# Optimization experiments

Hardware: AMD Instinct MI355X
Metric: run time of the kernel (lower is better)

## Reference

```python
import jax, jax.numpy as jnp
import numpy as np

B, S, D, H = 2, 2048, 1024, 16
HD = D // H
SCALE = float(np.sqrt(HD))


def setup_inputs() -> dict:
    key = jax.random.key(0)
    ks = jax.random.split(key, 11)
    std = 1.0 / np.sqrt(D)
    inp = {
        "query": jax.random.normal(ks[0], (B, S, D), dtype=jnp.float32),
        "key": jax.random.normal(ks[1], (B, S, D), dtype=jnp.float32),
        "value": jax.random.normal(ks[2], (B, S, D), dtype=jnp.float32),
        "w_q": jax.random.normal(ks[3], (D, D), dtype=jnp.float32) * std,
        "b_q": jax.random.normal(ks[4], (D,), dtype=jnp.float32) * std,
        "w_k": jax.random.normal(ks[5], (D, D), dtype=jnp.float32) * std,
        "b_k": jax.random.normal(ks[6], (D,), dtype=jnp.float32) * std,
        "w_v": jax.random.normal(ks[7], (D, D), dtype=jnp.float32) * std,
        "b_v": jax.random.normal(ks[8], (D,), dtype=jnp.float32) * std,
        "w_fc": jax.random.normal(ks[9], (D, D), dtype=jnp.float32) * std,
        "b_fc": jax.random.normal(ks[10], (D,), dtype=jnp.float32) * std,
    }
    return inp


def reference(query, key, value, w_q, b_q, w_k, b_k, w_v, b_v, w_fc, b_fc):
    # Linear projections (torch Linear: x @ W^T + b; here w_* stored as [in, out])
    Q = query @ w_q + b_q            # [B, S, D]
    K = key @ w_k + b_k
    V = value @ w_v + b_v
    # split heads -> [B, H, S, HD]
    Q = Q.reshape(B, S, H, HD).transpose(0, 2, 1, 3)
    K = K.reshape(B, S, H, HD).transpose(0, 2, 1, 3)
    V = V.reshape(B, S, H, HD).transpose(0, 2, 1, 3)
    energy = jnp.einsum('bhqd,bhkd->bhqk', Q, K) / SCALE  # [B, H, S, S]
    attn = jax.nn.softmax(energy, axis=-1)
    x = jnp.einsum('bhqk,bhkd->bhqd', attn, V)            # [B, H, S, HD]
    x = x.transpose(0, 2, 1, 3).reshape(B, S, D)
    return x @ w_fc + b_fc
```

## Files before the change

kernel.cpp:

```cpp
#include <hip/hip_runtime.h>
#include <stdint.h>

#define Bz 2
#define Sz 2048
#define Dz 1024
#define Hz 16
#define HDz 64
#define Mz (Bz*Sz)

typedef unsigned short u16;
typedef __attribute__((ext_vector_type(8))) __bf16 bf16x8;
typedef __attribute__((ext_vector_type(8))) unsigned short u16x8;
typedef __attribute__((ext_vector_type(4))) float f32x4;

#define C1 0.1803368801111243f

__device__ __forceinline__ u16 f2bf(float f) {
  union { float f; unsigned u; } v; v.f = f;
  unsigned r = v.u + 0x7fffu + ((v.u >> 16) & 1u);
  return (u16)(r >> 16);
}

__device__ __forceinline__ void async16(void* lds, const void* g) {
  __builtin_amdgcn_global_load_lds(
      (const __attribute__((address_space(1))) unsigned int*)g,
      (__attribute__((address_space(3))) unsigned int*)lds, 16, 0, 0);
}

__global__ void cvt3_kernel(const float* __restrict__ q, const float* __restrict__ k,
                            const float* __restrict__ v,
                            u16* __restrict__ xq, u16* __restrict__ xk, u16* __restrict__ xv,
                            int n4) {
  const float* in = blockIdx.y == 0 ? q : blockIdx.y == 1 ? k : v;
  u16* out = blockIdx.y == 0 ? xq : blockIdx.y == 1 ? xk : xv;
  int i = blockIdx.x * blockDim.x + threadIdx.x;
  if (i < n4) {
    float4 t = ((const float4*)in)[i];
    ((ushort4*)out)[i] = make_ushort4(f2bf(t.x), f2bf(t.y), f2bf(t.z), f2bf(t.w));
  }
}

__global__ void wt_cvt_kernel(const float* __restrict__ w0, const float* __restrict__ w1,
                              const float* __restrict__ w2, const float* __restrict__ w3,
                              u16* __restrict__ Wt ) {
  const float* W = blockIdx.z == 0 ? w0 : blockIdx.z == 1 ? w1 : blockIdx.z == 2 ? w2 : w3;
  u16* o = Wt + (size_t)blockIdx.z * Dz * Dz;
  __shared__ __align__(16) float t[32][33];
  int n0 = blockIdx.x * 32, k0 = blockIdx.y * 32;
  int x = threadIdx.x, y = threadIdx.y;
#pragma unroll
  for (int i = 0; i < 4; ++i)
    t[y + i*8][x] = W[(size_t)(k0 + y + i*8) * Dz + n0 + x];
  __syncthreads();
#pragma unroll
  for (int i = 0; i < 4; ++i)
    o[(size_t)(n0 + y + i*8) * Dz + k0 + x] = f2bf(t[x][y + i*8]);
}

__global__ void __launch_bounds__(256)
vtrans_kernel(const u16* __restrict__ Vp, u16* __restrict__ Vt) {
  __shared__ __align__(16) u16 t[64][72];
  int s0 = blockIdx.x * 64, bh = blockIdx.y;
  int b = bh >> 4;
  int h = bh & 15;
  int tid = threadIdx.x;
#pragma unroll
  for (int p = 0; p < 4; ++p) {
    int c = p * 256 + tid;
    int row = c >> 4, off = (c & 15) * 4;
    ushort4 v = *(const ushort4*)(Vp + (size_t)(b * Sz + s0 + row) * Dz + h * 64 + off);
    *(ushort4*)&t[row][off] = v;
  }
  __syncthreads();
#pragma unroll
  for (int p = 0; p < 4; ++p) {
    int c = p * 256 + tid;
    int d = c >> 4, sc = (c & 15) * 4;
    ushort4 v = make_ushort4(t[sc + 0][d], t[sc + 1][d], t[sc + 2][d], t[sc + 3][d]);
    *(ushort4*)(Vt + (size_t)(bh * 64 + d) * Sz + s0 + sc) = v;
  }
}

__global__ void __launch_bounds__(256)
gemm_qkv(const u16* __restrict__ xq, const u16* __restrict__ xk, const u16* __restrict__ xv,
         const u16* __restrict__ Wt3,
         const float* __restrict__ bq, const float* __restrict__ bk, const float* __restrict__ bv,
         u16* __restrict__ Qp, u16* __restrict__ Kp, u16* __restrict__ Vp)
{
  __shared__ __align__(16) u16 lA[128][32];
  __shared__ __align__(16) u16 lB[128][32];
  const int sel = blockIdx.x >> 3;
  const int n0 = (blockIdx.x & 7) * 128;
  const int m0 = blockIdx.y * 128;
  const u16* A = sel == 0 ? xq : sel == 1 ? xk : xv;
  const u16* Bt = Wt3 + (size_t)sel * Dz * Dz;
  const float* bias = sel == 0 ? bq : sel == 1 ? bk : bv;
  u16* Cv = sel == 0 ? Qp : sel == 1 ? Kp : Vp;

  const int tid = threadIdx.x;
  const int w = tid >> 6, lane = tid & 63;
  const int wm = (w >> 1) * 64, wn = (w & 1) * 64;
  const int l16 = lane & 15, qd = lane >> 4;

  f32x4 acc[4][4];
#pragma unroll
  for (int i = 0; i < 4; ++i)
#pragma unroll
    for (int j = 0; j < 4; ++j) acc[i][j] = (f32x4){0.f, 0.f, 0.f, 0.f};

  const int r0 = tid >> 2, c0 = (tid & 3) * 8;
  const int r1 = r0 + 64;

  for (int k0 = 0; k0 < Dz; k0 += 32) {
    __syncthreads();
    async16(&lA[r0][c0], A  + (size_t)(m0 + r0) * Dz + k0 + c0);
    async16(&lB[r0][c0], Bt + (size_t)(n0 + r0) * Dz + k0 + c0);
    async16(&lA[r1][c0], A  + (size_t)(m0 + r1) * Dz + k0 + c0);
    async16(&lB[r1][c0], Bt + (size_t)(n0 + r1) * Dz + k0 + c0);
    __syncthreads();
    bf16x8 af[4], bfv[4];
#pragma unroll
    for (int t = 0; t < 4; ++t) {
      af[t]  = *(const bf16x8*)&lA[wm + t * 16 + l16][qd * 8];
      bfv[t] = *(const bf16x8*)&lB[wn + t * 16 + l16][qd * 8];
    }
#pragma unroll
    for (int mt = 0; mt < 4; ++mt)
#pragma unroll
      for (int nt = 0; nt < 4; ++nt)
        acc[mt][nt] = __builtin_amdgcn_mfma_f32_16x16x32_bf16(af[mt], bfv[nt], acc[mt][nt], 0, 0, 0);
  }

#pragma unroll
  for (int nt = 0; nt < 4; ++nt) {
    const int n = n0 + wn + nt * 16 + l16;
    const float bvl = bias[n];
#pragma unroll
    for (int mt = 0; mt < 4; ++mt)
#pragma unroll
      for (int r = 0; r < 4; ++r) {
        const int m = m0 + wm + mt * 16 + qd * 4 + r;
        Cv[(size_t)m * Dz + n] = f2bf(acc[mt][nt][r] + bvl);
      }
  }
}

__global__ void __launch_bounds__(256)
gemm_fc(const u16* __restrict__ A, const u16* __restrict__ Bt,
        const float* __restrict__ bias, float* __restrict__ C)
{
  __shared__ __align__(16) u16 lA[128][32];
  __shared__ __align__(16) u16 lB[64][32];
  const int m0 = blockIdx.y * 128, n0 = blockIdx.x * 64;
  const int tid = threadIdx.x;
  const int w = tid >> 6, lane = tid & 63;
  const int wm = (w >> 1) * 64, wn = (w & 1) * 32;
  const int l16 = lane & 15, qd = lane >> 4;

  f32x4 acc[4][2];
#pragma unroll
  for (int i = 0; i < 4; ++i)
#pragma unroll
    for (int j = 0; j < 2; ++j) acc[i][j] = (f32x4){0.f, 0.f, 0.f, 0.f};

  const int r0 = tid >> 2, c0 = (tid & 3) * 8;

  for (int k0 = 0; k0 < Dz; k0 += 32) {
    __syncthreads();
    async16(&lA[r0][c0],      A  + (size_t)(m0 + r0) * Dz + k0 + c0);
    async16(&lA[r0 + 64][c0], A  + (size_t)(m0 + r0 + 64) * Dz + k0 + c0);
    async16(&lB[r0][c0],      Bt + (size_t)(n0 + r0) * Dz + k0 + c0);
    __syncthreads();
    bf16x8 af[4], bfv[2];
#pragma unroll
    for (int t = 0; t < 4; ++t)
      af[t] = *(const bf16x8*)&lA[wm + t * 16 + l16][qd * 8];
#pragma unroll
    for (int t = 0; t < 2; ++t)
      bfv[t] = *(const bf16x8*)&lB[wn + t * 16 + l16][qd * 8];
#pragma unroll
    for (int mt = 0; mt < 4; ++mt)
#pragma unroll
      for (int nt = 0; nt < 2; ++nt)
        acc[mt][nt] = __builtin_amdgcn_mfma_f32_16x16x32_bf16(af[mt], bfv[nt], acc[mt][nt], 0, 0, 0);
  }

#pragma unroll
  for (int nt = 0; nt < 2; ++nt) {
    const int n = n0 + wn + nt * 16 + l16;
    const float bvl = bias[n];
#pragma unroll
    for (int mt = 0; mt < 4; ++mt)
#pragma unroll
      for (int r = 0; r < 4; ++r) {
        const int m = m0 + wm + mt * 16 + qd * 4 + r;
        C[(size_t)m * Dz + n] = acc[mt][nt][r] + bvl;
      }
  }
}

__global__ void __launch_bounds__(256, 2)
attn_kernel(const u16* __restrict__ Qp, const u16* __restrict__ Kp,
            const u16* __restrict__ Vt, u16* __restrict__ Ao)
{
  __shared__ __align__(16) u16 lK[128][72];
  __shared__ __align__(16) u16 lV[64][136];
  __shared__ __align__(16) u16 lP[4][32][136];

  const int q0 = blockIdx.x * 128;
  const int bh = blockIdx.y;
  const int b = bh >> 4, h = bh & 15;
  const int tid = threadIdx.x, w = tid >> 6, lane = tid & 63;
  const int l16 = lane & 15, qd = lane >> 4;

  const int krow = tid >> 3, kcol = (tid & 7) * 8;
  const int vrow = tid >> 4, vcol = (tid & 15) * 8;

  u16x8 kreg[4], vreg[4];
#pragma unroll
  for (int p = 0; p < 4; ++p) {
    kreg[p] = *(const u16x8*)(Kp + (size_t)(b * Sz + p * 32 + krow) * Dz + h * 64 + kcol);
    vreg[p] = *(const u16x8*)(Vt + (size_t)(bh * 64 + p * 16 + vrow) * Sz + vcol);
  }

  bf16x8 qf[2][2];
#pragma unroll
  for (int mt = 0; mt < 2; ++mt)
#pragma unroll
    for (int ks = 0; ks < 2; ++ks)
      qf[mt][ks] = *(const bf16x8*)(Qp + (size_t)(b * Sz + q0 + w * 32 + mt * 16 + l16) * Dz
                                    + h * 64 + ks * 32 + qd * 8);

  u16x8 ob;
#pragma unroll
  for (int i = 0; i < 8; ++i) ob[i] = 0x3F80u;
  const bf16x8 onesf = __builtin_bit_cast(bf16x8, ob);

  f32x4 oacc[2][4], lacc[2];
#pragma unroll
  for (int i = 0; i < 2; ++i) {
    lacc[i] = (f32x4){0.f, 0.f, 0.f, 0.f};
#pragma unroll
    for (int j = 0; j < 4; ++j) oacc[i][j] = (f32x4){0.f, 0.f, 0.f, 0.f};
  }

  for (int t = 0; t < Sz / 128; ++t) {
    __syncthreads();
#pragma unroll
    for (int p = 0; p < 4; ++p) {
      *(u16x8*)&lK[p * 32 + krow][kcol] = kreg[p];
      *(u16x8*)&lV[p * 16 + vrow][vcol] = vreg[p];
    }
    if (t + 1 < Sz / 128) {
      const int kv = (t + 1) * 128;
#pragma unroll
      for (int p = 0; p < 4; ++p) {
        kreg[p] = *(const u16x8*)(Kp + (size_t)(b * Sz + kv + p * 32 + krow) * Dz + h * 64 + kcol);
        vreg[p] = *(const u16x8*)(Vt + (size_t)(bh * 64 + p * 16 + vrow) * Sz + kv + vcol);
      }
    }
    __syncthreads();

    f32x4 sacc[2][8];
#pragma unroll
    for (int i = 0; i < 2; ++i)
#pragma unroll
      for (int j = 0; j < 8; ++j) sacc[i][j] = (f32x4){0.f, 0.f, 0.f, 0.f};
#pragma unroll
    for (int ks = 0; ks < 2; ++ks) {
      bf16x8 bfv[8];
#pragma unroll
      for (int nt = 0; nt < 8; ++nt)
        bfv[nt] = *(const bf16x8*)&lK[nt * 16 + l16][ks * 32 + qd * 8];
#pragma unroll
      for (int mt = 0; mt < 2; ++mt)
#pragma unroll
        for (int nt = 0; nt < 8; ++nt)
          sacc[mt][nt] = __builtin_amdgcn_mfma_f32_16x16x32_bf16(qf[mt][ks], bfv[nt], sacc[mt][nt], 0, 0, 0);
    }

#pragma unroll
    for (int mt = 0; mt < 2; ++mt)
#pragma unroll
      for (int nt = 0; nt < 8; ++nt)
#pragma unroll
        for (int r = 0; r < 4; ++r) {
          float pv = exp2f(sacc[mt][nt][r] * C1);
          unsigned bits = __builtin_bit_cast(unsigned, pv);
          lP[w][mt * 16 + qd * 4 + r][nt * 16 + l16] = (u16)((bits + 0x8000u) >> 16);
        }

#pragma unroll
    for (int ks = 0; ks < 4; ++ks) {
      bf16x8 pa[2], vb[4];
      pa[0] = *(const bf16x8*)&lP[w][l16     ][ks * 32 + qd * 8];
      pa[1] = *(const bf16x8*)&lP[w][16 + l16][ks * 32 + qd * 8];
#pragma unroll
      for (int nt = 0; nt < 4; ++nt)
        vb[nt] = *(const bf16x8*)&lV[nt * 16 + l16][ks * 32 + qd * 8];
#pragma unroll
      for (int mt = 0; mt < 2; ++mt) {
#pragma unroll
        for (int nt = 0; nt < 4; ++nt)
          oacc[mt][nt] = __builtin_amdgcn_mfma_f32_16x16x32_bf16(pa[mt], vb[nt], oacc[mt][nt], 0, 0, 0);
        lacc[mt] = __builtin_amdgcn_mfma_f32_16x16x32_bf16(pa[mt], onesf, lacc[mt], 0, 0, 0);
      }
    }
  }

#pragma unroll
  for (int mt = 0; mt < 2; ++mt)
#pragma unroll
    for (int r = 0; r < 4; ++r) {
      const float inv = 1.0f / lacc[mt][r];
      const int row = q0 + w * 32 + mt * 16 + qd * 4 + r;
#pragma unroll
      for (int nt = 0; nt < 4; ++nt) {
        const int col = h * 64 + nt * 16 + l16;
        Ao[(size_t)(b * Sz + row) * Dz + col] = f2bf(oacc[mt][nt][r] * inv);
      }
    }
}

extern "C" void kernel_launch(void* const* d_in, const int* in_sizes, int n_in,
                              void* d_out, int out_size, void* d_ws, size_t ws_size,
                              hipStream_t stream) {
  const float* query = (const float*)d_in[0];
  const float* key   = (const float*)d_in[1];
  const float* value = (const float*)d_in[2];
  const float* w_q  = (const float*)d_in[3];
  const float* b_q  = (const float*)d_in[4];
  const float* w_k  = (const float*)d_in[5];
  const float* b_k  = (const float*)d_in[6];
  const float* w_v  = (const float*)d_in[7];
  const float* b_v  = (const float*)d_in[8];
  const float* w_fc = (const float*)d_in[9];
  const float* b_fc = (const float*)d_in[10];
  float* out = (float*)d_out;

  const size_t XE = (size_t)Mz * Dz;
  const size_t WE = (size_t)Dz * Dz;
  u16* Xq  = (u16*)d_ws;
  u16* Xk  = Xq + XE;
  u16* Xv  = Xk + XE;
  u16* Wt  = Xv + XE;
  u16* Wtf = Wt + 3 * WE;
  u16* Qp  = Wt + 4 * WE;
  u16* Kp  = Qp + XE;
  u16* Vp  = Kp + XE;
  u16* Vt  = Xk;
  u16* Ao  = Xq;

  const int n4 = (int)(XE / 4);
  cvt3_kernel<<<dim3(n4 / 256, 3), 256, 0, stream>>>(query, key, value, Xq, Xk, Xv, n4);

  wt_cvt_kernel<<<dim3(Dz / 32, Dz / 32, 4), dim3(32, 8), 0, stream>>>(w_q, w_k, w_v, w_fc, Wt);

  gemm_qkv<<<dim3(24, Mz / 128), 256, 0, stream>>>(Xq, Xk, Xv, Wt, b_q, b_k, b_v, Qp, Kp, Vp);

  vtrans_kernel<<<dim3(Sz / 64, Bz * Hz), 256, 0, stream>>>(Vp, Vt);

  attn_kernel<<<dim3(Sz / 128, Bz * Hz), 256, 0, stream>>>(Qp, Kp, Vt, Ao);

  gemm_fc<<<dim3(Dz / 64, Mz / 128), 256, 0, stream>>>(Ao, Wtf, b_fc, out);
}
```

Baseline: 252.7 us.

## Merge prep kernels, write V transposed from QKV GEMM, transpose score MFMA

Combines the activation-convert and weight-transpose kernels into one launch, and removes the separate V transpose kernel by having the QKV GEMM write V directly in head-transposed layout. It also swaps the operand order of the QK^T MFMA so each lane holds four consecutive key positions, which lets the probabilities be packed and stored to LDS as 8-byte vectors instead of scalar 2-byte stores. The goal is fewer launches, one fewer global round-trip over V, and fewer LDS store instructions. The risk is more divergence in the merged prep kernel and strided global stores in the V epilogue.

Result: slower. 259.5 us (+2.7%).

```diff
diff --git a/kernel.cpp b/kernel.cpp
--- a/kernel.cpp
+++ b/kernel.cpp
@@ -21,63 +21,47 @@
   return (u16)(r >> 16);
 }
 
+__device__ __forceinline__ unsigned packbf(float a, float b) {
+  unsigned ua = __builtin_bit_cast(unsigned, a);
+  unsigned ub = __builtin_bit_cast(unsigned, b);
+  return ((ua + 0x8000u) >> 16) | ((ub + 0x8000u) & 0xFFFF0000u);
+}
+
 __device__ __forceinline__ void async16(void* lds, const void* g) {
   __builtin_amdgcn_global_load_lds(
       (const __attribute__((address_space(1))) unsigned int*)g,
       (__attribute__((address_space(3))) unsigned int*)lds, 16, 0, 0);
 }
 
-__global__ void cvt3_kernel(const float* __restrict__ q, const float* __restrict__ k,
-                            const float* __restrict__ v,
-                            u16* __restrict__ xq, u16* __restrict__ xk, u16* __restrict__ xv,
-                            int n4) {
-  const float* in = blockIdx.y == 0 ? q : blockIdx.y == 1 ? k : v;
-  u16* out = blockIdx.y == 0 ? xq : blockIdx.y == 1 ? xk : xv;
-  int i = blockIdx.x * blockDim.x + threadIdx.x;
-  if (i < n4) {
-    float4 t = ((const float4*)in)[i];
-    ((ushort4*)out)[i] = make_ushort4(f2bf(t.x), f2bf(t.y), f2bf(t.z), f2bf(t.w));
-  }
-}
-
-__global__ void wt_cvt_kernel(const float* __restrict__ w0, const float* __restrict__ w1,
-                              const float* __restrict__ w2, const float* __restrict__ w3,
-                              u16* __restrict__ Wt ) {
-  const float* W = blockIdx.z == 0 ? w0 : blockIdx.z == 1 ? w1 : blockIdx.z == 2 ? w2 : w3;
-  u16* o = Wt + (size_t)blockIdx.z * Dz * Dz;
+__global__ void __launch_bounds__(256)
+prep_kernel(const float* __restrict__ q, const float* __restrict__ k, const float* __restrict__ v,
+            const float* __restrict__ w0, const float* __restrict__ w1,
+            const float* __restrict__ w2, const float* __restrict__ w3,
+            u16* __restrict__ xq, u16* __restrict__ xk, u16* __restrict__ xv,
+            u16* __restrict__ Wt) {
   __shared__ __align__(16) float t[32][33];
-  int n0 = blockIdx.x * 32, k0 = blockIdx.y * 32;
-  int x = threadIdx.x, y = threadIdx.y;
-#pragma unroll
-  for (int i = 0; i < 4; ++i)
-    t[y + i*8][x] = W[(size_t)(k0 + y + i*8) * Dz + n0 + x];
-  __syncthreads();
-#pragma unroll
-  for (int i = 0; i < 4; ++i)
-    o[(size_t)(n0 + y + i*8) * Dz + k0 + x] = f2bf(t[x][y + i*8]);
-}
-
-__global__ void __launch_bounds__(256)
-vtrans_kernel(const u16* __restrict__ Vp, u16* __restrict__ Vt) {
-  __shared__ __align__(16) u16 t[64][72];
-  int s0 = blockIdx.x * 64, bh = blockIdx.y;
-  int b = bh >> 4;
-  int h = bh & 15;
-  int tid = threadIdx.x;
-#pragma unroll
-  for (int p = 0; p < 4; ++p) {
-    int c = p * 256 + tid;
-    int row = c >> 4, off = (c & 15) * 4;
-    ushort4 v = *(const ushort4*)(Vp + (size_t)(b * Sz + s0 + row) * Dz + h * 64 + off);
-    *(ushort4*)&t[row][off] = v;
-  }
-  __syncthreads();
-#pragma unroll
-  for (int p = 0; p < 4; ++p) {
-    int c = p * 256 + tid;
-    int d = c >> 4, sc = (c & 15) * 4;
-    ushort4 v = make_ushort4(t[sc + 0][d], t[sc + 1][d], t[sc + 2][d], t[sc + 3][d]);
-    *(ushort4*)(Vt + (size_t)(bh * 64 + d) * Sz + s0 + sc) = v;
+  const int bid = blockIdx.x, tid = threadIdx.x;
+  if (bid < 12288) {
+    const int sel = bid >> 12;
+    const int i = ((bid & 4095) << 8) + tid;
+    const float* in = sel == 0 ? q : sel == 1 ? k : v;
+    u16* out = sel == 0 ? xq : sel == 1 ? xk : xv;
+    float4 tv = ((const float4*)in)[i];
+    ((ushort4*)out)[i] = make_ushort4(f2bf(tv.x), f2bf(tv.y), f2bf(tv.z), f2bf(tv.w));
+  } else {
+    const int idx = bid - 12288;
+    const int z = idx >> 10, r = idx & 1023;
+    const int n0 = (r & 31) * 32, k0 = (r >> 5) * 32;
+    const float* W = z == 0 ? w0 : z == 1 ? w1 : z == 2 ? w2 : w3;
+    u16* o = Wt + (size_t)z * Dz * Dz;
+    const int x = tid & 31, y = tid >> 5;
+#pragma unroll
+    for (int i = 0; i < 4; ++i)
+      t[y + i*8][x] = W[(size_t)(k0 + y + i*8) * Dz + n0 + x];
+    __syncthreads();
+#pragma unroll
+    for (int i = 0; i < 4; ++i)
+      o[(size_t)(n0 + y + i*8) * Dz + k0 + x] = f2bf(t[x][y + i*8]);
   }
 }
 
@@ -85,7 +69,7 @@
 gemm_qkv(const u16* __restrict__ xq, const u16* __restrict__ xk, const u16* __restrict__ xv,
          const u16* __restrict__ Wt3,
          const float* __restrict__ bq, const float* __restrict__ bk, const float* __restrict__ bv,
-         u16* __restrict__ Qp, u16* __restrict__ Kp, u16* __restrict__ Vp)
+         u16* __restrict__ Qp, u16* __restrict__ Kp, u16* __restrict__ Vt)
 {
   __shared__ __align__(16) u16 lA[128][32];
   __shared__ __align__(16) u16 lB[128][32];
@@ -95,7 +79,6 @@
   const u16* A = sel == 0 ? xq : sel == 1 ? xk : xv;
   const u16* Bt = Wt3 + (size_t)sel * Dz * Dz;
   const float* bias = sel == 0 ? bq : sel == 1 ? bk : bv;
-  u16* Cv = sel == 0 ? Qp : sel == 1 ? Kp : Vp;
 
   const int tid = threadIdx.x;
   const int w = tid >> 6, lane = tid & 63;
@@ -131,17 +114,37 @@
         acc[mt][nt] = __builtin_amdgcn_mfma_f32_16x16x32_bf16(af[mt], bfv[nt], acc[mt][nt], 0, 0, 0);
   }
 
-#pragma unroll
-  for (int nt = 0; nt < 4; ++nt) {
-    const int n = n0 + wn + nt * 16 + l16;
-    const float bvl = bias[n];
-#pragma unroll
-    for (int mt = 0; mt < 4; ++mt)
-#pragma unroll
-      for (int r = 0; r < 4; ++r) {
-        const int m = m0 + wm + mt * 16 + qd * 4 + r;
-        Cv[(size_t)m * Dz + n] = f2bf(acc[mt][nt][r] + bvl);
-      }
+  if (sel == 2) {
+    const int bq2 = m0 >> 11;
+    const int s0m = (m0 & 2047) + wm;
+#pragma unroll
+    for (int nt = 0; nt < 4; ++nt) {
+      const int n = n0 + wn + nt * 16 + l16;
+      const float bvl = bias[n];
+      const int h = n >> 6, hd = n & 63;
+      u16* vp = Vt + (size_t)((bq2 * 16 + h) * 64 + hd) * Sz;
+#pragma unroll
+      for (int mt = 0; mt < 4; ++mt) {
+        const int s = s0m + mt * 16 + qd * 4;
+        ushort4 o = make_ushort4(f2bf(acc[mt][nt][0] + bvl), f2bf(acc[mt][nt][1] + bvl),
+                                 f2bf(acc[mt][nt][2] + bvl), f2bf(acc[mt][nt][3] + bvl));
+        *(ushort4*)(vp + s) = o;
+      }
+    }
+  } else {
+    u16* Cv = sel == 0 ? Qp : Kp;
+#pragma unroll
+    for (int nt = 0; nt < 4; ++nt) {
+      const int n = n0 + wn + nt * 16 + l16;
+      const float bvl = bias[n];
+#pragma unroll
+      for (int mt = 0; mt < 4; ++mt)
+#pragma unroll
+        for (int r = 0; r < 4; ++r) {
+          const int m = m0 + wm + mt * 16 + qd * 4 + r;
+          Cv[(size_t)m * Dz + n] = f2bf(acc[mt][nt][r] + bvl);
+        }
+    }
   }
 }
 
@@ -225,11 +228,11 @@
 
   bf16x8 qf[2][2];
 #pragma unroll
-  for (int mt = 0; mt < 2; ++mt)
-#pragma unroll
-    for (int ks = 0; ks < 2; ++ks)
-      qf[mt][ks] = *(const bf16x8*)(Qp + (size_t)(b * Sz + q0 + w * 32 + mt * 16 + l16) * Dz
-                                    + h * 64 + ks * 32 + qd * 8);
+  for (int qt = 0; qt < 2; ++qt)
+#pragma unroll
+    for (int ksd = 0; ksd < 2; ++ksd)
+      qf[qt][ksd] = *(const bf16x8*)(Qp + (size_t)(b * Sz + q0 + w * 32 + qt * 16 + l16) * Dz
+                                     + h * 64 + ksd * 32 + qd * 8);
 
   u16x8 ob;
 #pragma unroll
@@ -261,34 +264,37 @@
     }
     __syncthreads();
 
-    f32x4 sacc[2][8];
-#pragma unroll
-    for (int i = 0; i < 2; ++i)
-#pragma unroll
-      for (int j = 0; j < 8; ++j) sacc[i][j] = (f32x4){0.f, 0.f, 0.f, 0.f};
-#pragma unroll
-    for (int ks = 0; ks < 2; ++ks) {
-      bf16x8 bfv[8];
-#pragma unroll
-      for (int nt = 0; nt < 8; ++nt)
-        bfv[nt] = *(const bf16x8*)&lK[nt * 16 + l16][ks * 32 + qd * 8];
-#pragma unroll
-      for (int mt = 0; mt < 2; ++mt)
-#pragma unroll
-        for (int nt = 0; nt < 8; ++nt)
-          sacc[mt][nt] = __builtin_amdgcn_mfma_f32_16x16x32_bf16(qf[mt][ks], bfv[nt], sacc[mt][nt], 0, 0, 0);
-    }
-
-#pragma unroll
-    for (int mt = 0; mt < 2; ++mt)
-#pragma unroll
-      for (int nt = 0; nt < 8; ++nt)
-#pragma unroll
-        for (int r = 0; r < 4; ++r) {
-          float pv = exp2f(sacc[mt][nt][r] * C1);
-          unsigned bits = __builtin_bit_cast(unsigned, pv);
-          lP[w][mt * 16 + qd * 4 + r][nt * 16 + l16] = (u16)((bits + 0x8000u) >> 16);
-        }
+    f32x4 st[8][2];
+#pragma unroll
+    for (int i = 0; i < 8; ++i)
+#pragma unroll
+      for (int j = 0; j < 2; ++j) st[i][j] = (f32x4){0.f, 0.f, 0.f, 0.f};
+#pragma unroll
+    for (int ksd = 0; ksd < 2; ++ksd) {
+      bf16x8 kf[8];
+#pragma unroll
+      for (int kvt = 0; kvt < 8; ++kvt)
+        kf[kvt] = *(const bf16x8*)&lK[kvt * 16 + l16][ksd * 32 + qd * 8];
+#pragma unroll
+      for (int kvt = 0; kvt < 8; ++kvt)
+#pragma unroll
+        for (int qt = 0; qt < 2; ++qt)
+          st[kvt][qt] = __builtin_amdgcn_mfma_f32_16x16x32_bf16(kf[kvt], qf[qt][ksd], st[kvt][qt], 0, 0, 0);
+    }
+
+#pragma unroll
+    for (int kvt = 0; kvt < 8; ++kvt)
+#pragma unroll
+      for (int qt = 0; qt < 2; ++qt) {
+        float e0 = exp2f(st[kvt][qt][0] * C1);
+        float e1 = exp2f(st[kvt][qt][1] * C1);
+        float e2 = exp2f(st[kvt][qt][2] * C1);
+        float e3 = exp2f(st[kvt][qt][3] * C1);
+        uint2 pk;
+        pk.x = packbf(e0, e1);
+        pk.y = packbf(e2, e3);
+        *(uint2*)&lP[w][qt * 16 + l16][kvt * 16 + qd * 4] = pk;
+      }
 
 #pragma unroll
     for (int ks = 0; ks < 4; ++ks) {
@@ -347,18 +353,13 @@
   u16* Wtf = Wt + 3 * WE;
   u16* Qp  = Wt + 4 * WE;
   u16* Kp  = Qp + XE;
-  u16* Vp  = Kp + XE;
-  u16* Vt  = Xk;
+  u16* Vt  = Kp + XE;
   u16* Ao  = Xq;
 
-  const int n4 = (int)(XE / 4);
-  cvt3_kernel<<<dim3(n4 / 256, 3), 256, 0, stream>>>(query, key, value, Xq, Xk, Xv, n4);
-
-  wt_cvt_kernel<<<dim3(Dz / 32, Dz / 32, 4), dim3(32, 8), 0, stream>>>(w_q, w_k, w_v, w_fc, Wt);
-
-  gemm_qkv<<<dim3(24, Mz / 128), 256, 0, stream>>>(Xq, Xk, Xv, Wt, b_q, b_k, b_v, Qp, Kp, Vp);
-
-  vtrans_kernel<<<dim3(Sz / 64, Bz * Hz), 256, 0, stream>>>(Vp, Vt);
+  prep_kernel<<<16384, 256, 0, stream>>>(query, key, value, w_q, w_k, w_v, w_fc,
+                                         Xq, Xk, Xv, Wt);
+
+  gemm_qkv<<<dim3(24, Mz / 128), 256, 0, stream>>>(Xq, Xk, Xv, Wt, b_q, b_k, b_v, Qp, Kp, Vt);
 
   attn_kernel<<<dim3(Sz / 128, Bz * Hz), 256, 0, stream>>>(Qp, Kp, Vt, Ao);
 
```
